# Performance work log

Hardware: AMD Instinct MI355X
Metric: run time of the kernel (lower is better)

The kernel has to match this reference:

```python
import jax, jax.numpy as jnp
import numpy as np

CONF = 2.5  # confidence threshold from init_kwargs
N, C = 300000, 80

def setup_inputs() -> dict:
    key = jax.random.key(0)
    k1, k2 = jax.random.split(key)
    post_result = jax.random.normal(k1, (N, C), dtype=jnp.float32)
    pre_post_boxes = jax.random.normal(k2, (N, 4), dtype=jnp.float32)
    return {"post_result": post_result, "pre_post_boxes": pre_post_boxes}

def reference(post_result, pre_post_boxes):
    # per-box max over classes: [N]
    m = jnp.max(post_result, axis=1)
    mask = m >= CONF  # [N] bool
    # ouput_type == 'all': sum of passing maxes + sum of their 4 box coords
    score_sum = jnp.sum(jnp.where(mask, m, 0.0))
    box_sum = jnp.sum(jnp.where(mask[:, None], pre_post_boxes, 0.0))
    return score_sum + box_sum
```

## Files before the change

kernel.cpp:

```cpp
#include <hip/hip_runtime.h>

#define CONF_THR 2.5f
#define NCLS 80
#define BLOCK 256
#define ITERS 2
#define ROWS_PER_BLOCK (64 * ITERS)

__global__ __launch_bounds__(BLOCK, 8) void yolo_pass1(
    const float* __restrict__ post,
    const float* __restrict__ boxes,
    float* __restrict__ partial, int n) {

    const int tid  = threadIdx.x;
    const int lane = tid & 63;
    const int wav  = tid >> 6;
    const int q    = tid & 3;
    const int sub  = tid >> 2;
    const int base = blockIdx.x * ROWS_PER_BLOCK;

    float4 v[ITERS][5];
    float  bx[ITERS];

    #pragma unroll
    for (int it = 0; it < ITERS; ++it) {
        const int row = base + it * 64 + sub;
        if (row < n) {
            const float4* p = reinterpret_cast<const float4*>(
                post + (size_t)row * NCLS + q * 20);
            bx[it] = boxes[(size_t)row * 4 + q];
            v[it][0] = p[0]; v[it][1] = p[1]; v[it][2] = p[2];
            v[it][3] = p[3]; v[it][4] = p[4];
        } else {
            const float4 ninf = make_float4(-1e30f, -1e30f, -1e30f, -1e30f);
            v[it][0] = ninf; v[it][1] = ninf; v[it][2] = ninf;
            v[it][3] = ninf; v[it][4] = ninf;
            bx[it] = 0.0f;
        }
    }

    float c = 0.0f;
    #pragma unroll
    for (int it = 0; it < ITERS; ++it) {
        float m0 = fmaxf(fmaxf(v[it][0].x, v[it][0].y), fmaxf(v[it][0].z, v[it][0].w));
        float m1 = fmaxf(fmaxf(v[it][1].x, v[it][1].y), fmaxf(v[it][1].z, v[it][1].w));
        float m2 = fmaxf(fmaxf(v[it][2].x, v[it][2].y), fmaxf(v[it][2].z, v[it][2].w));
        float m3 = fmaxf(fmaxf(v[it][3].x, v[it][3].y), fmaxf(v[it][3].z, v[it][3].w));
        float m4 = fmaxf(fmaxf(v[it][4].x, v[it][4].y), fmaxf(v[it][4].z, v[it][4].w));
        float m  = fmaxf(fmaxf(fmaxf(m0, m1), fmaxf(m2, m3)), m4);
        m = fmaxf(m, __shfl_xor(m, 1));
        m = fmaxf(m, __shfl_xor(m, 2));
        if (m >= CONF_THR) c += bx[it] + ((q == 0) ? m : 0.0f);
    }

    #pragma unroll
    for (int off = 1; off < 64; off <<= 1)
        c += __shfl_xor(c, off);

    __shared__ float ws[4];
    if (lane == 0) ws[wav] = c;
    __syncthreads();
    if (tid == 0) partial[blockIdx.x] = ws[0] + ws[1] + ws[2] + ws[3];
}

__global__ __launch_bounds__(1024) void yolo_pass2(
    const float* __restrict__ partial, float* __restrict__ out, int nb) {

    const int tid  = threadIdx.x;
    const int lane = tid & 63;
    const int wav  = tid >> 6;

    float s = 0.0f;
    for (int i = tid; i < nb; i += 1024) s += partial[i];

    #pragma unroll
    for (int off = 1; off < 64; off <<= 1)
        s += __shfl_xor(s, off);

    __shared__ float ws[16];
    if (lane == 0) ws[wav] = s;
    __syncthreads();
    if (tid == 0) {
        float t = 0.0f;
        #pragma unroll
        for (int w = 0; w < 16; ++w) t += ws[w];
        out[0] = t;
    }
}

extern "C" void kernel_launch(void* const* d_in, const int* in_sizes, int n_in,
                              void* d_out, int out_size, void* d_ws, size_t ws_size,
                              hipStream_t stream) {
    const float* post  = (const float*)d_in[0];
    const float* boxes = (const float*)d_in[1];
    float* out     = (float*)d_out;
    float* partial = (float*)d_ws;

    const int n  = in_sizes[0] / NCLS;
    const int nb = (n + ROWS_PER_BLOCK - 1) / ROWS_PER_BLOCK;

    yolo_pass1<<<nb, BLOCK, 0, stream>>>(post, boxes, partial, n);
    yolo_pass2<<<1, 1024, 0, stream>>>(partial, out, nb);
}
```

Before: 22.47 us.

## Use fully coalesced float4 loads with LDS staging for per-row max

Replaces the per-row strided float4 loads, where each lane read a 20-float chunk of one row, with contiguous wave-wide float4 loads across the flat post_result buffer. Partial maxima go to shared memory, and 32 lanes then finish the row maxima, which are broadcast with shuffles for thresholding. Box loads also become contiguous per wave. This aims to improve memory coalescing, at the cost of extra LDS traffic and an uneven second reduction stage where only half the lanes work.

New measurement: 31.40 us. +39.8%, slower.

```diff
diff --git a/kernel.cpp b/kernel.cpp
--- a/kernel.cpp
+++ b/kernel.cpp
@@ -3,8 +3,9 @@
 #define CONF_THR 2.5f
 #define NCLS 80
 #define BLOCK 256
-#define ITERS 2
-#define ROWS_PER_BLOCK (64 * ITERS)
+#define ROWS_PER_STEP 64
+#define STEPS_PER_BLOCK 2
+#define ROWS_PER_BLOCK (ROWS_PER_STEP * STEPS_PER_BLOCK)
 
 __global__ __launch_bounds__(BLOCK, 8) void yolo_pass1(
     const float* __restrict__ post,
@@ -14,52 +15,70 @@
     const int tid  = threadIdx.x;
     const int lane = tid & 63;
     const int wav  = tid >> 6;
-    const int q    = tid & 3;
-    const int sub  = tid >> 2;
-    const int base = blockIdx.x * ROWS_PER_BLOCK;
+    const long nfloat4 = (long)n * (NCLS / 4);
 
-    float4 v[ITERS][5];
-    float  bx[ITERS];
+    const int s0 = blockIdx.x * STEPS_PER_BLOCK;
+
+    __shared__ float smax[4][STEPS_PER_BLOCK][320];
+    __shared__ float wsum[4];
+
+    const float4* post4 = reinterpret_cast<const float4*>(post);
+    const float4 ninf = make_float4(-1e30f, -1e30f, -1e30f, -1e30f);
+
+    float4 v[STEPS_PER_BLOCK][5];
+    float  bx[STEPS_PER_BLOCK];
+    #pragma unroll
+    for (int s = 0; s < STEPS_PER_BLOCK; ++s) {
+        const long F = (long)(s0 + s) * 1280 + wav * 320;
+        #pragma unroll
+        for (int i = 0; i < 5; ++i) {
+            const long idx = F + i * 64 + lane;
+            v[s][i] = (idx < nfloat4) ? post4[idx] : ninf;
+        }
+        const int rbase = (s0 + s) * ROWS_PER_STEP + wav * 16;
+        const int brow  = rbase + (lane >> 2);
+        bx[s] = (brow < n) ? boxes[(size_t)rbase * 4 + lane] : 0.0f;
+    }
 
     #pragma unroll
-    for (int it = 0; it < ITERS; ++it) {
-        const int row = base + it * 64 + sub;
-        if (row < n) {
-            const float4* p = reinterpret_cast<const float4*>(
-                post + (size_t)row * NCLS + q * 20);
-            bx[it] = boxes[(size_t)row * 4 + q];
-            v[it][0] = p[0]; v[it][1] = p[1]; v[it][2] = p[2];
-            v[it][3] = p[3]; v[it][4] = p[4];
-        } else {
-            const float4 ninf = make_float4(-1e30f, -1e30f, -1e30f, -1e30f);
-            v[it][0] = ninf; v[it][1] = ninf; v[it][2] = ninf;
-            v[it][3] = ninf; v[it][4] = ninf;
-            bx[it] = 0.0f;
+    for (int s = 0; s < STEPS_PER_BLOCK; ++s) {
+        #pragma unroll
+        for (int i = 0; i < 5; ++i) {
+            float m = fmaxf(fmaxf(v[s][i].x, v[s][i].y),
+                            fmaxf(v[s][i].z, v[s][i].w));
+            smax[wav][s][i * 64 + lane] = m;
         }
     }
 
+    float rowmax = -1e30f;
+    {
+        const int s = (lane >> 4) & 1;
+        const int r = lane & 15;
+        if (lane < 32) {
+            const float4* p = reinterpret_cast<const float4*>(&smax[wav][s][r * 20]);
+            float4 a0 = p[0], a1 = p[1], a2 = p[2], a3 = p[3], a4 = p[4];
+            float m0 = fmaxf(fmaxf(a0.x, a0.y), fmaxf(a0.z, a0.w));
+            float m1 = fmaxf(fmaxf(a1.x, a1.y), fmaxf(a1.z, a1.w));
+            float m2 = fmaxf(fmaxf(a2.x, a2.y), fmaxf(a2.z, a2.w));
+            float m3 = fmaxf(fmaxf(a3.x, a3.y), fmaxf(a3.z, a3.w));
+            float m4 = fmaxf(fmaxf(a4.x, a4.y), fmaxf(a4.z, a4.w));
+            rowmax = fmaxf(fmaxf(fmaxf(m0, m1), fmaxf(m2, m3)), m4);
+        }
+    }
+
+    const float m0 = __shfl(rowmax, lane >> 2);
+    const float m1 = __shfl(rowmax, 16 + (lane >> 2));
     float c = 0.0f;
-    #pragma unroll
-    for (int it = 0; it < ITERS; ++it) {
-        float m0 = fmaxf(fmaxf(v[it][0].x, v[it][0].y), fmaxf(v[it][0].z, v[it][0].w));
-        float m1 = fmaxf(fmaxf(v[it][1].x, v[it][1].y), fmaxf(v[it][1].z, v[it][1].w));
-        float m2 = fmaxf(fmaxf(v[it][2].x, v[it][2].y), fmaxf(v[it][2].z, v[it][2].w));
-        float m3 = fmaxf(fmaxf(v[it][3].x, v[it][3].y), fmaxf(v[it][3].z, v[it][3].w));
-        float m4 = fmaxf(fmaxf(v[it][4].x, v[it][4].y), fmaxf(v[it][4].z, v[it][4].w));
-        float m  = fmaxf(fmaxf(fmaxf(m0, m1), fmaxf(m2, m3)), m4);
-        m = fmaxf(m, __shfl_xor(m, 1));
-        m = fmaxf(m, __shfl_xor(m, 2));
-        if (m >= CONF_THR) c += bx[it] + ((q == 0) ? m : 0.0f);
-    }
+    if (m0 >= CONF_THR) c += bx[0] + (((lane & 3) == 0) ? m0 : 0.0f);
+    if (m1 >= CONF_THR) c += bx[1] + (((lane & 3) == 0) ? m1 : 0.0f);
 
     #pragma unroll
     for (int off = 1; off < 64; off <<= 1)
         c += __shfl_xor(c, off);
 
-    __shared__ float ws[4];
-    if (lane == 0) ws[wav] = c;
+    if (lane == 0) wsum[wav] = c;
     __syncthreads();
-    if (tid == 0) partial[blockIdx.x] = ws[0] + ws[1] + ws[2] + ws[3];
+    if (tid == 0) partial[blockIdx.x] = wsum[0] + wsum[1] + wsum[2] + wsum[3];
 }
 
 __global__ __launch_bounds__(1024) void yolo_pass2(
```
